# Kernel tuning notes

Hardware: AMD Instinct MI355X
Metric: run time of the kernel (lower is better)

Reference implementation:

```python
import jax, jax.numpy as jnp
import numpy as np

EPS = 1e-8  # torch.nn.CosineSimilarity default eps


def setup_inputs() -> dict:
    key = jax.random.key(0)
    H, W, C = 1024, 1024, 128
    input_image = jax.random.normal(key, (H, W, 1, C), dtype=jnp.float32)
    return {"input_image": input_image}


def reference(input_image):
    # input_image: [H, W, 1, C]; cosine similarity of each pixel with its
    # valid 3x3 neighbors (including self), summed, minus 1 (the self term).
    x = input_image[:, :, 0, :]  # [H, W, C]
    H, W, _ = x.shape
    # torch cosine: dot(a,b) / (max(||a||,eps) * max(||b||,eps))
    # = dot(a/max(||a||,eps), b/max(||b||,eps)) -> normalize once.
    norm = jnp.sqrt(jnp.sum(x * x, axis=-1, keepdims=True))
    xn = x / jnp.maximum(norm, EPS)  # [H, W, C]
    # zero-pad by 1; zero rows/cols contribute 0 == out-of-range mask in original
    xp = jnp.pad(xn, ((1, 1), (1, 1), (0, 0)))  # [H+2, W+2, C]
    sim = jnp.zeros((H, W), dtype=x.dtype)
    for k in (-1, 0, 1):
        for l in (-1, 0, 1):
            shifted = jax.lax.dynamic_slice(xp, (1 + k, 1 + l, 0), (H, W, xp.shape[-1]))
            sim = sim + jnp.einsum('hwc,hwc->hw', xn, shifted)
    return sim - 1.0
```

## Files before the change

### kernel.cpp

```cpp
#include <hip/hip_runtime.h>


#define HH 1024
#define WW 1024
#define C4 32
#define SOUT 64
#define SHALO (SOUT + 2)
#define RROWS 32
#define NT 512
#define NSTAGE ((SHALO * C4 + NT - 1) / NT)
#define OWN ((SOUT * C4) / NT)

__device__ __forceinline__ float dot4(float4 a, float4 b) {
    return fmaf(a.x, b.x, fmaf(a.y, b.y, fmaf(a.z, b.z, a.w * b.w)));
}

__device__ __forceinline__ void stage_row(const float4* __restrict__ in,
                                          int y, int x0, int t, bool need,
                                          float4 (&v)[NSTAGE]) {
#pragma unroll
    for (int i = 0; i < NSTAGE; ++i) {
        const int idx = t + i * NT;
        float4 val = make_float4(0.f, 0.f, 0.f, 0.f);
        const bool inR = (i < NSTAGE - 1) || (idx < SHALO * C4);
        if (inR) {
            const int gx = x0 - 1 + (idx >> 5);
            if (need && gx >= 0 && gx < WW) {
                val = in[(size_t)(y * WW + gx) * C4 + (idx & 31)];
            }
        }
        v[i] = val;
    }
}

__global__ __launch_bounds__(NT, 4)
void cos_sim_kernel(const float4* __restrict__ in, float* __restrict__ out) {
    __shared__ float4 xrow[2][SHALO * C4];

    const int t   = threadIdx.x;
    const int c4  = t & 31;
    const int xo0 = t >> 5;
    const int x0  = blockIdx.x * SOUT;
    const int r0  = blockIdx.y * RROWS;
    const int ylast = r0 + RROWS;

    float4 Hprev[OWN], XNprev[OWN];
    float  accP[OWN];
#pragma unroll
    for (int i = 0; i < OWN; ++i) {
        Hprev[i]  = make_float4(0.f, 0.f, 0.f, 0.f);
        XNprev[i] = make_float4(0.f, 0.f, 0.f, 0.f);
        accP[i]   = 0.f;
    }

    float4 vA[NSTAGE], vB[NSTAGE];
    stage_row(in, r0 - 1, x0, t, (r0 - 1 >= 0), vA);

    int buf = 0;
    for (int y = r0 - 1; y <= ylast; ++y) {
        const int yn = y + 1;
        stage_row(in, yn, x0, t,
                  (yn >= 0) && (yn < HH) && (yn <= ylast), vB);

#pragma unroll
        for (int i = 0; i < NSTAGE; ++i) {
            const int idx = t + i * NT;
            float s = dot4(vA[i], vA[i]);
            s += __shfl_xor(s, 1);
            s += __shfl_xor(s, 2);
            s += __shfl_xor(s, 4);
            s += __shfl_xor(s, 8);
            s += __shfl_xor(s, 16);
            const float inv = rsqrtf(fmaxf(s, 1e-16f));
            const bool inR = (i < NSTAGE - 1) || (idx < SHALO * C4);
            if (inR) {
                float4 w;
                w.x = vA[i].x * inv; w.y = vA[i].y * inv;
                w.z = vA[i].z * inv; w.w = vA[i].w * inv;
                xrow[buf][idx] = w;
            }
        }

        asm volatile("s_waitcnt lgkmcnt(0)" ::: "memory");
        __builtin_amdgcn_s_barrier();

#pragma unroll
        for (int i = 0; i < OWN; ++i) {
            const int xo = xo0 + 16 * i;
            const float4 a = xrow[buf][(xo    ) * C4 + c4];
            const float4 b = xrow[buf][(xo + 1) * C4 + c4];
            const float4 r = xrow[buf][(xo + 2) * C4 + c4];
            float4 Hc;
            Hc.x = a.x + b.x + r.x; Hc.y = a.y + b.y + r.y;
            Hc.z = a.z + b.z + r.z; Hc.w = a.w + b.w + r.w;

            float fin = accP[i] + dot4(XNprev[i], Hc);
            accP[i]   = dot4(b, Hprev[i]) + dot4(b, Hc);
            XNprev[i] = b;
            Hprev[i]  = Hc;

            if (y > r0) {
                fin += __shfl_xor(fin, 1);
                fin += __shfl_xor(fin, 2);
                fin += __shfl_xor(fin, 4);
                fin += __shfl_xor(fin, 8);
                fin += __shfl_xor(fin, 16);
                if (c4 == 0) {
                    out[(size_t)(y - 1) * WW + x0 + xo] = fin - 1.0f;
                }
            }
        }

        buf ^= 1;
#pragma unroll
        for (int i = 0; i < NSTAGE; ++i) vA[i] = vB[i];
    }
}

extern "C" void kernel_launch(void* const* d_in, const int* in_sizes, int n_in,
                              void* d_out, int out_size, void* d_ws, size_t ws_size,
                              hipStream_t stream) {
    const float4* in = (const float4*)d_in[0];
    float* out = (float*)d_out;
    dim3 grid(WW / SOUT, HH / RROWS);
    cos_sim_kernel<<<grid, NT, 0, stream>>>(in, out);
}
```

Before: 699.5 us.

## Replace LDS-tiled row pipeline with per-wave register streaming and global halo loads

The shared-memory double-buffered tile and block barrier are removed. Each wave now owns two output columns and streams down a 64-row segment, loading the left, center and right neighbor pixels directly from global memory into registers, with a two-row prefetch. Every pixel is re-normalized three times and read three times from global memory, relying on L2/cache to absorb the horizontal halo reuse. Block IDs are remapped in an XCD-aware order, and the block size drops to 256 with a higher occupancy hint.

```diff
diff --git a/kernel.cpp b/kernel.cpp
--- a/kernel.cpp
+++ b/kernel.cpp
@@ -4,116 +4,98 @@
 #define HH 1024
 #define WW 1024
 #define C4 32
-#define SOUT 64
-#define SHALO (SOUT + 2)
-#define RROWS 32
-#define NT 512
-#define NSTAGE ((SHALO * C4 + NT - 1) / NT)
-#define OWN ((SOUT * C4) / NT)
+#define ROWF4 (WW * C4)
+#define SEGROWS 64
+#define NSEG (HH / SEGROWS)
+#define NT 256
+#define NBLK ((WW / 8) * NSEG)
 
 __device__ __forceinline__ float dot4(float4 a, float4 b) {
     return fmaf(a.x, b.x, fmaf(a.y, b.y, fmaf(a.z, b.z, a.w * b.w)));
 }
 
-__device__ __forceinline__ void stage_row(const float4* __restrict__ in,
-                                          int y, int x0, int t, bool need,
-                                          float4 (&v)[NSTAGE]) {
-#pragma unroll
-    for (int i = 0; i < NSTAGE; ++i) {
-        const int idx = t + i * NT;
-        float4 val = make_float4(0.f, 0.f, 0.f, 0.f);
-        const bool inR = (i < NSTAGE - 1) || (idx < SHALO * C4);
-        if (inR) {
-            const int gx = x0 - 1 + (idx >> 5);
-            if (need && gx >= 0 && gx < WW) {
-                val = in[(size_t)(y * WW + gx) * C4 + (idx & 31)];
-            }
-        }
-        v[i] = val;
-    }
+__device__ __forceinline__ float wsum32(float s) {
+    s += __shfl_xor(s, 1);
+    s += __shfl_xor(s, 2);
+    s += __shfl_xor(s, 4);
+    s += __shfl_xor(s, 8);
+    s += __shfl_xor(s, 16);
+    return s;
 }
 
-__global__ __launch_bounds__(NT, 4)
+__global__ __launch_bounds__(NT, 6)
 void cos_sim_kernel(const float4* __restrict__ in, float* __restrict__ out) {
-    __shared__ float4 xrow[2][SHALO * C4];
+    const int tid  = threadIdx.x;
+    const int lane = tid & 63;
+    const int wv   = tid >> 6;
+    const int cl   = lane & 31;
+    const int hf   = lane >> 5;
 
-    const int t   = threadIdx.x;
-    const int c4  = t & 31;
-    const int xo0 = t >> 5;
-    const int x0  = blockIdx.x * SOUT;
-    const int r0  = blockIdx.y * RROWS;
-    const int ylast = r0 + RROWS;
+    const int bid = blockIdx.x;
+    const int lg  = (bid & 7) * (NBLK / 8) + (bid >> 3);
+    const int colgrp = lg & 127;
+    const int yseg   = lg >> 7;
 
-    float4 Hprev[OWN], XNprev[OWN];
-    float  accP[OWN];
-#pragma unroll
-    for (int i = 0; i < OWN; ++i) {
-        Hprev[i]  = make_float4(0.f, 0.f, 0.f, 0.f);
-        XNprev[i] = make_float4(0.f, 0.f, 0.f, 0.f);
-        accP[i]   = 0.f;
-    }
+    const int x0    = colgrp * 8 + wv * 2;
+    const int rbase = yseg * SEGROWS;
+    const int ymax  = min(rbase + SEGROWS, HH - 1);
 
-    float4 vA[NSTAGE], vB[NSTAGE];
-    stage_row(in, r0 - 1, x0, t, (r0 - 1 >= 0), vA);
+    const int xL = x0 - 1 + hf;
+    const int xR = x0 + 1 + hf;
+    const bool okL = (xL >= 0);
+    const bool okR = (xR < WW);
+    const int offL = max(xL, 0) * C4 + cl;
+    const int offC = (x0 + hf) * C4 + cl;
+    const int offR = min(xR, WW - 1) * C4 + cl;
 
-    int buf = 0;
-    for (int y = r0 - 1; y <= ylast; ++y) {
-        const int yn = y + 1;
-        stage_row(in, yn, x0, t,
-                  (yn >= 0) && (yn < HH) && (yn <= ylast), vB);
+    float4 XNp = make_float4(0.f, 0.f, 0.f, 0.f);
+    float4 Hp  = make_float4(0.f, 0.f, 0.f, 0.f);
+    float  accP = 0.f;
 
-#pragma unroll
-        for (int i = 0; i < NSTAGE; ++i) {
-            const int idx = t + i * NT;
-            float s = dot4(vA[i], vA[i]);
-            s += __shfl_xor(s, 1);
-            s += __shfl_xor(s, 2);
-            s += __shfl_xor(s, 4);
-            s += __shfl_xor(s, 8);
-            s += __shfl_xor(s, 16);
-            const float inv = rsqrtf(fmaxf(s, 1e-16f));
-            const bool inR = (i < NSTAGE - 1) || (idx < SHALO * C4);
-            if (inR) {
-                float4 w;
-                w.x = vA[i].x * inv; w.y = vA[i].y * inv;
-                w.z = vA[i].z * inv; w.w = vA[i].w * inv;
-                xrow[buf][idx] = w;
+    const size_t pb0 = (size_t)max(rbase - 1, 0) * ROWF4;
+    const size_t pb1 = (size_t)rbase * ROWF4;
+    float4 l0 = in[pb0 + offL], c0 = in[pb0 + offC], q0 = in[pb0 + offR];
+    float4 l1 = in[pb1 + offL], c1 = in[pb1 + offC], q1 = in[pb1 + offR];
+
+#pragma unroll 2
+    for (int i = 0; i < SEGROWS + 2; ++i) {
+        const int y  = rbase - 1 + i;
+        const int yp = min(y + 2, ymax);
+        const size_t pb = (size_t)yp * ROWF4;
+        float4 nl = in[pb + offL];
+        float4 nc = in[pb + offC];
+        float4 nr = in[pb + offR];
+
+        const bool oky = (y >= 0) && (y < HH);
+        const float4 Z = make_float4(0.f, 0.f, 0.f, 0.f);
+        const float4 L = (oky && okL) ? l0 : Z;
+        const float4 Cc = oky ? c0 : Z;
+        const float4 R = (oky && okR) ? q0 : Z;
+
+        const float iL = rsqrtf(fmaxf(wsum32(dot4(L, L)),   1e-16f));
+        const float iC = rsqrtf(fmaxf(wsum32(dot4(Cc, Cc)), 1e-16f));
+        const float iR = rsqrtf(fmaxf(wsum32(dot4(R, R)),   1e-16f));
+
+        float4 xc, H;
+        xc.x = Cc.x * iC; xc.y = Cc.y * iC; xc.z = Cc.z * iC; xc.w = Cc.w * iC;
+        H.x = fmaf(L.x, iL, fmaf(R.x, iR, xc.x));
+        H.y = fmaf(L.y, iL, fmaf(R.y, iR, xc.y));
+        H.z = fmaf(L.z, iL, fmaf(R.z, iR, xc.z));
+        H.w = fmaf(L.w, iL, fmaf(R.w, iR, xc.w));
+
+        float fin = accP + dot4(XNp, H);
+        accP = dot4(xc, Hp) + dot4(xc, H);
+        XNp = xc; Hp = H;
+
+        if (y > rbase) {
+            fin = wsum32(fin);
+            if (cl == 0) {
+                out[(size_t)(y - 1) * WW + x0 + hf] = fin - 1.0f;
             }
         }
 
-        asm volatile("s_waitcnt lgkmcnt(0)" ::: "memory");
-        __builtin_amdgcn_s_barrier();
-
-#pragma unroll
-        for (int i = 0; i < OWN; ++i) {
-            const int xo = xo0 + 16 * i;
-            const float4 a = xrow[buf][(xo    ) * C4 + c4];
-            const float4 b = xrow[buf][(xo + 1) * C4 + c4];
-            const float4 r = xrow[buf][(xo + 2) * C4 + c4];
-            float4 Hc;
-            Hc.x = a.x + b.x + r.x; Hc.y = a.y + b.y + r.y;
-            Hc.z = a.z + b.z + r.z; Hc.w = a.w + b.w + r.w;
-
-            float fin = accP[i] + dot4(XNprev[i], Hc);
-            accP[i]   = dot4(b, Hprev[i]) + dot4(b, Hc);
-            XNprev[i] = b;
-            Hprev[i]  = Hc;
-
-            if (y > r0) {
-                fin += __shfl_xor(fin, 1);
-                fin += __shfl_xor(fin, 2);
-                fin += __shfl_xor(fin, 4);
-                fin += __shfl_xor(fin, 8);
-                fin += __shfl_xor(fin, 16);
-                if (c4 == 0) {
-                    out[(size_t)(y - 1) * WW + x0 + xo] = fin - 1.0f;
-                }
-            }
-        }
-
-        buf ^= 1;
-#pragma unroll
-        for (int i = 0; i < NSTAGE; ++i) vA[i] = vB[i];
+        l0 = l1; c0 = c1; q0 = q1;
+        l1 = nl; c1 = nc; q1 = nr;
     }
 }
 
@@ -122,6 +104,5 @@
                               hipStream_t stream) {
     const float4* in = (const float4*)d_in[0];
     float* out = (float*)d_out;
-    dim3 grid(WW / SOUT, HH / RROWS);
-    cos_sim_kernel<<<grid, NT, 0, stream>>>(in, out);
+    cos_sim_kernel<<<dim3(NBLK), dim3(NT), 0, stream>>>(in, out);
 }
```

New measurement: 712.6 us. Within noise of the previous version (+1.9%).
